# Kernel optimization log

Hardware: AMD Instinct MI355X
Metric: run time of the kernel (lower is better)

## Reference

```python
import jax, jax.numpy as jnp
import numpy as np

D_MODEL = 1024
D_STATE = 16
EXPAND = 2
D_CONV = 4
D_INNER = EXPAND * D_MODEL          # 2048
DT_RANK = D_MODEL // 16             # 64
B = 2
L = 1024
EPS = 1e-5


def setup_inputs() -> dict:
    key = jax.random.key(0)
    ks = jax.random.split(key, 8)
    s = 0.02
    return {
        "x": jax.random.normal(ks[0], (B, L, D_MODEL), jnp.float32),
        "ln_gamma": jnp.ones((D_MODEL,), jnp.float32),
        "ln_beta": jnp.zeros((D_MODEL,), jnp.float32),
        "in_proj_w": jax.random.normal(ks[1], (2 * D_INNER, D_MODEL), jnp.float32) * s,
        "conv_w": jax.random.normal(ks[2], (D_INNER, 1, D_CONV), jnp.float32) * s,
        "conv_b": jnp.zeros((D_INNER,), jnp.float32),
        "x_proj_w": jax.random.normal(ks[3], (DT_RANK + 2 * D_STATE, D_INNER), jnp.float32) * s,
        "dt_proj_w": jax.random.normal(ks[4], (D_INNER, DT_RANK), jnp.float32) * s,
        "dt_proj_b": jax.random.normal(ks[5], (D_INNER,), jnp.float32) * 0.01,
        "A_log": jnp.log(jnp.tile(jnp.arange(1, D_STATE + 1, dtype=jnp.float32), (D_INNER, 1))),
        "D_skip": jnp.ones((D_INNER,), jnp.float32),
        "out_proj_w": jax.random.normal(ks[6], (D_MODEL, D_INNER), jnp.float32) * s,
    }


def _layernorm(x, g, b):
    mu = jnp.mean(x, axis=-1, keepdims=True)
    var = jnp.mean((x - mu) ** 2, axis=-1, keepdims=True)
    return (x - mu) * jax.lax.rsqrt(var + EPS) * g + b


def _mamba_forward(x, ln_gamma, ln_beta, in_proj_w, conv_w, conv_b,
                   x_proj_w, dt_proj_w, dt_proj_b, A_log, D_skip, out_proj_w):
    residual = x
    xn = _layernorm(x, ln_gamma, ln_beta)

    # in_proj -> split into ssm input u and gate z   (b, l, 2*d_inner)
    xz = jnp.einsum('bld,ed->ble', xn, in_proj_w)
    u, z = jnp.split(xz, 2, axis=-1)

    # causal depthwise conv1d (padding = d_conv-1 on the left, truncated to L)
    uc = jnp.transpose(u, (0, 2, 1))  # (b, d_inner, l)
    uc = jax.lax.conv_general_dilated(
        uc, conv_w, window_strides=(1,), padding=[(D_CONV - 1, 0)],
        feature_group_count=D_INNER,
        dimension_numbers=('NCH', 'OIH', 'NCH'))
    uc = uc + conv_b[None, :, None]
    u = jax.nn.silu(jnp.transpose(uc, (0, 2, 1)))  # (b, l, d_inner)

    # selective SSM
    A = -jnp.exp(A_log)                              # (d_inner, d_state)
    x_dbl = jnp.einsum('bld,ed->ble', u, x_proj_w)   # (b, l, dt_rank+2*n)
    dt, Bm, Cm = jnp.split(x_dbl, [DT_RANK, DT_RANK + D_STATE], axis=-1)
    delta = jax.nn.softplus(jnp.einsum('blr,dr->bld', dt, dt_proj_w) + dt_proj_b)

    def step(h, inputs):
        d_t, B_t, C_t, u_t = inputs            # (b,di) (b,n) (b,n) (b,di)
        dA = jnp.exp(d_t[..., None] * A)       # (b, di, n)
        h = dA * h + (d_t * u_t)[..., None] * B_t[:, None, :]
        y = jnp.einsum('bdn,bn->bd', h, C_t)
        return h, y

    h0 = jnp.zeros((x.shape[0], D_INNER, D_STATE), x.dtype)
    xs = (jnp.moveaxis(delta, 1, 0), jnp.moveaxis(Bm, 1, 0),
          jnp.moveaxis(Cm, 1, 0), jnp.moveaxis(u, 1, 0))
    _, ys = jax.lax.scan(step, h0, xs)
    y = jnp.moveaxis(ys, 0, 1) + u * D_skip     # (b, l, d_inner)

    y = y * jax.nn.silu(z)                      # gated output
    out = jnp.einsum('ble,de->bld', y, out_proj_w)
    # dropout is identity in eval mode
    return out + residual


def reference(x, ln_gamma, ln_beta, in_proj_w, conv_w, conv_b,
              x_proj_w, dt_proj_w, dt_proj_b, A_log, D_skip, out_proj_w):
    return _mamba_forward(x, ln_gamma, ln_beta, in_proj_w, conv_w, conv_b,
                          x_proj_w, dt_proj_w, dt_proj_b, A_log, D_skip, out_proj_w)
```

## Files before the change

kernel.cpp:

```cpp
#include <hip/hip_runtime.h>

#define D_MODEL 1024
#define D_STATE 16
#define D_INNER 2048
#define DT_RANK 64
#define NBATCH 2
#define SEQ_L 1024
#define M_ROWS (NBATCH * SEQ_L)
#define CHUNK 32
#define NCHUNK (SEQ_L / CHUNK)

typedef __bf16 bf16x8 __attribute__((ext_vector_type(8)));
typedef float f32x4 __attribute__((ext_vector_type(4)));
typedef unsigned short u16;
typedef unsigned int u32;

__device__ __forceinline__ float bf2f(u16 h) {
    return __uint_as_float(((unsigned)h) << 16);
}
__device__ __forceinline__ u16 f2bf(float f) {
    unsigned u = __float_as_uint(f);
    u += 0x7fff + ((u >> 16) & 1);
    return (u16)(u >> 16);
}

__global__ __launch_bounds__(256) void prep(
    const float* __restrict__ s0, const float* __restrict__ s1,
    const float* __restrict__ s2, const float* __restrict__ s3,
    u16* __restrict__ d0, u16* __restrict__ d1,
    u16* __restrict__ d2, u16* __restrict__ d3,
    const float* __restrict__ x, const float* __restrict__ g,
    const float* __restrict__ b, u16* __restrict__ xn) {
    int blk = blockIdx.x;
    if (blk < 25856) {
        int idx = blk * 256 + threadIdx.x;
        if (idx < 4194304) {
            d0[idx] = f2bf(s0[idx]);
        } else if (idx < 6291456) {
            int i = idx - 4194304; d1[i] = f2bf(s1[i]);
        } else if (idx < 6488064) {
            int i = idx - 6291456; d2[i] = f2bf(s2[i]);
        } else {
            int i = idx - 6488064; d3[i] = f2bf(s3[i]);
        }
        return;
    }
    int row = blk - 25856;
    const float4* xr = (const float4*)(x + (size_t)row * D_MODEL);
    float4 v = xr[threadIdx.x];
    float s  = v.x + v.y + v.z + v.w;
    float ss = v.x * v.x + v.y * v.y + v.z * v.z + v.w * v.w;
#pragma unroll
    for (int off = 32; off > 0; off >>= 1) {
        s  += __shfl_down(s,  off, 64);
        ss += __shfl_down(ss, off, 64);
    }
    __shared__ float sh_s[4], sh_ss[4];
    int wid = threadIdx.x >> 6;
    if ((threadIdx.x & 63) == 0) { sh_s[wid] = s; sh_ss[wid] = ss; }
    __syncthreads();
    float mu  = (sh_s[0] + sh_s[1] + sh_s[2] + sh_s[3]) * (1.0f / D_MODEL);
    float var = (sh_ss[0] + sh_ss[1] + sh_ss[2] + sh_ss[3]) * (1.0f / D_MODEL) - mu * mu;
    float rs = rsqrtf(var + 1e-5f);
    int c0 = threadIdx.x * 4;
    float vv[4] = {v.x, v.y, v.z, v.w};
#pragma unroll
    for (int j = 0; j < 4; j++) {
        int c = c0 + j;
        float o = (vv[j] - mu) * rs * g[c] + b[c];
        xn[(size_t)row * D_MODEL + c] = f2bf(o);
    }
}

template <int BM, int BN, int WM, int WN, int MODE>
__global__ __launch_bounds__(256) void gemm_lds(
    const __bf16* __restrict__ A, const __bf16* __restrict__ W,
    int K, int Ksteps, int ldC,
    float* __restrict__ outF, u16* __restrict__ outB) {
    constexpr int WCOLS = BN / (WN * 16);
    __shared__ __bf16 As[BM * 32];
    __shared__ __bf16 Bs[BN * 32];
    int tid  = threadIdx.x;
    int lane = tid & 63;
    int wid  = tid >> 6;
    int l16  = lane & 15;
    int quad = lane >> 4;
    int wr = wid / WCOLS;
    int wc = wid % WCOLS;
    int m0 = blockIdx.y * BM;
    int n0 = blockIdx.x * BN;
    int kbase = blockIdx.z * Ksteps * 32;

    f32x4 acc[WM][WN];
#pragma unroll
    for (int mi = 0; mi < WM; mi++)
#pragma unroll
        for (int nj = 0; nj < WN; nj++)
            acc[mi][nj] = (f32x4){0.f, 0.f, 0.f, 0.f};

    for (int ki = 0; ki < Ksteps; ki++) {
        int k0 = kbase + ki * 32;
        __syncthreads();
#pragma unroll
        for (int i = 0; i < BM / 64; i++) {
            int t   = i * 256 + tid;
            int row = t >> 2;
            int cg  = (t & 3) ^ ((row >> 1) & 3);
            __builtin_amdgcn_global_load_lds(
                (const __attribute__((address_space(1))) u32*)(A + (size_t)(m0 + row) * K + k0 + cg * 8),
                (__attribute__((address_space(3))) u32*)(As + (i * 256 + wid * 64) * 8),
                16, 0, 0);
        }
#pragma unroll
        for (int i = 0; i < BN / 64; i++) {
            int t   = i * 256 + tid;
            int row = t >> 2;
            int cg  = (t & 3) ^ ((row >> 1) & 3);
            __builtin_amdgcn_global_load_lds(
                (const __attribute__((address_space(1))) u32*)(W + (size_t)(n0 + row) * K + k0 + cg * 8),
                (__attribute__((address_space(3))) u32*)(Bs + (i * 256 + wid * 64) * 8),
                16, 0, 0);
        }
        __syncthreads();

        bf16x8 af[WM], bfr[WN];
#pragma unroll
        for (int mi = 0; mi < WM; mi++) {
            int r  = wr * WM * 16 + mi * 16 + l16;
            int cg = quad ^ ((r >> 1) & 3);
            af[mi] = *(const bf16x8*)(As + r * 32 + cg * 8);
        }
#pragma unroll
        for (int nj = 0; nj < WN; nj++) {
            int r  = wc * WN * 16 + nj * 16 + l16;
            int cg = quad ^ ((r >> 1) & 3);
            bfr[nj] = *(const bf16x8*)(Bs + r * 32 + cg * 8);
        }
#pragma unroll
        for (int mi = 0; mi < WM; mi++)
#pragma unroll
            for (int nj = 0; nj < WN; nj++)
                acc[mi][nj] = __builtin_amdgcn_mfma_f32_16x16x32_bf16(
                    af[mi], bfr[nj], acc[mi][nj], 0, 0, 0);
    }

    float* outP = (MODE == 4) ? outF + (size_t)blockIdx.z * M_ROWS * ldC : outF;
#pragma unroll
    for (int mi = 0; mi < WM; mi++) {
#pragma unroll
        for (int nj = 0; nj < WN; nj++) {
            int col = n0 + wc * WN * 16 + nj * 16 + l16;
#pragma unroll
            for (int r = 0; r < 4; r++) {
                int row = m0 + wr * WM * 16 + mi * 16 + quad * 4 + r;
                float v = acc[mi][nj][r];
                if (MODE == 0) {
                    outB[(size_t)row * ldC + col] = f2bf(v);
                } else {
                    outP[(size_t)row * ldC + col] = v;
                }
            }
        }
    }
}

__global__ __launch_bounds__(256) void out_reduce(
    const float* __restrict__ p, const float* __restrict__ x,
    float* __restrict__ out) {
    int idx = blockIdx.x * 256 + threadIdx.x;
    const int N = M_ROWS * D_MODEL;
    float4 a = ((const float4*)p)[idx];
    float4 b = ((const float4*)(p + N))[idx];
    float4 c = ((const float4*)(p + 2 * N))[idx];
    float4 d = ((const float4*)(p + 3 * N))[idx];
    float4 r = ((const float4*)x)[idx];
    float4 o;
    o.x = a.x + b.x + c.x + d.x + r.x;
    o.y = a.y + b.y + c.y + d.y + r.y;
    o.z = a.z + b.z + c.z + d.z + r.z;
    o.w = a.w + b.w + c.w + d.w + r.w;
    ((float4*)out)[idx] = o;
}

template <int MODE>
__global__ __launch_bounds__(256) void gemm_bt(
    const __bf16* __restrict__ A, const __bf16* __restrict__ W,
    int K, int Ksplit, int Nw, int ldC,
    float* __restrict__ outF, u16* __restrict__ outB16,
    const float* __restrict__ auxF) {
    int lane = threadIdx.x & 63;
    int wid  = threadIdx.x >> 6;
    int m0 = blockIdx.y * 64;
    int n0 = blockIdx.x * 64;
    int kc = blockIdx.z;
    int l16  = lane & 15;
    int quad = lane >> 4;
    int mrow = m0 + wid * 16 + l16;

    const __bf16* ap = A + (size_t)mrow * K + kc * Ksplit + quad * 8;
    const __bf16* wp[4];
#pragma unroll
    for (int j = 0; j < 4; j++) {
        int nc = n0 + j * 16 + l16;
        if (nc > Nw - 1) nc = Nw - 1;
        wp[j] = W + (size_t)nc * K + kc * Ksplit + quad * 8;
    }
    f32x4 acc[4];
#pragma unroll
    for (int j = 0; j < 4; j++) acc[j] = (f32x4){0.f, 0.f, 0.f, 0.f};

    for (int k = 0; k < Ksplit; k += 32) {
        bf16x8 a = *(const bf16x8*)ap;
        ap += 32;
#pragma unroll
        for (int j = 0; j < 4; j++) {
            bf16x8 bfr = *(const bf16x8*)wp[j];
            wp[j] += 32;
            acc[j] = __builtin_amdgcn_mfma_f32_16x16x32_bf16(a, bfr, acc[j], 0, 0, 0);
        }
    }
    float* out = (MODE == 1) ? outF + (size_t)kc * (M_ROWS * 96) : outF;
#pragma unroll
    for (int j = 0; j < 4; j++) {
        int col = n0 + j * 16 + l16;
#pragma unroll
        for (int r = 0; r < 4; r++) {
            int row = m0 + wid * 16 + quad * 4 + r;
            float v = acc[j][r];
            if (MODE == 1) {
                if (col < Nw) out[(size_t)row * ldC + col] = v;
            } else {
                float t = v + auxF[col];
                float sp = (t > 20.f) ? t : log1pf(__expf(t));
                outB16[(size_t)row * ldC + col] = f2bf(sp);
            }
        }
    }
}

__global__ __launch_bounds__(256) void xdbl_reduce(
    const float* __restrict__ xdp, float* __restrict__ xd,
    u16* __restrict__ dtb) {
    int idx = blockIdx.x * 256 + threadIdx.x;
    const int N = M_ROWS * 96;
    float v = 0.f;
#pragma unroll
    for (int i = 0; i < 8; i++) v += xdp[idx + i * N];
    xd[idx] = v;
    int mrow = idx / 96;
    int r = idx - mrow * 96;
    if (r < DT_RANK) dtb[mrow * DT_RANK + r] = f2bf(v);
}

__global__ __launch_bounds__(256) void conv_silu(
    const u16* __restrict__ xz, const float* __restrict__ cw,
    const float* __restrict__ cb, u16* __restrict__ uc) {
    int idx = blockIdx.x * 256 + threadIdx.x;
    int d = idx & (D_INNER - 1);
    int m = idx >> 11;
    int t = m & (SEQ_L - 1);
    float s = cb[d];
#pragma unroll
    for (int j = 0; j < 4; j++) {
        int tt = t - 3 + j;
        if (tt >= 0) {
            s += cw[d * 4 + j] *
                 bf2f(xz[(size_t)(m - 3 + j) * (2 * D_INNER) + d]);
        }
    }
    float sig = 1.f / (1.f + __expf(-s));
    uc[idx] = f2bf(s * sig);
}

__global__ __launch_bounds__(256) void scan_chunk(
    const u16* __restrict__ delta, const u16* __restrict__ uc,
    const float* __restrict__ xd, const float* __restrict__ A_log,
    float* __restrict__ Pst, float* __restrict__ Sst) {
    __shared__ float Bsh[CHUNK][16];
    int tid  = threadIdx.x;
    int lane = tid & 63;
    int w    = tid >> 6;
    int dsub = lane & 15;
    int g    = lane >> 4;
    int n0   = g * 4;
    int c = blockIdx.x, b = blockIdx.z;
    int d = blockIdx.y * 64 + w * 16 + dsub;
    int mbase = b * SEQ_L + c * CHUNK;

    if (tid < CHUNK * 4) {
        int row = tid >> 2, q = tid & 3;
        *(float4*)&Bsh[row][q * 4] =
            *(const float4*)(xd + (size_t)(mbase + row) * 96 + DT_RANK + q * 4);
    }
    __syncthreads();

    float a[4];
    {
        float4 a0 = *(const float4*)(A_log + d * D_STATE + n0);
        a[0] = -__expf(a0.x); a[1] = -__expf(a0.y);
        a[2] = -__expf(a0.z); a[3] = -__expf(a0.w);
    }
    float P[4] = {1.f, 1.f, 1.f, 1.f}, S[4] = {0.f, 0.f, 0.f, 0.f};

    for (int t0 = 0; t0 < CHUNK; t0 += 4) {
        float dlv[4], uv[4];
#pragma unroll
        for (int i = 0; i < 4; i++) {
            int m = mbase + t0 + i;
            dlv[i] = bf2f(delta[(size_t)m * D_INNER + d]);
            uv[i]  = bf2f(uc[(size_t)m * D_INNER + d]);
        }
#pragma unroll
        for (int i = 0; i < 4; i++) {
            float c1 = dlv[i] * uv[i];
#pragma unroll
            for (int j = 0; j < 4; j++) {
                float dA = __expf(dlv[i] * a[j]);
                P[j] *= dA;
                S[j] = dA * S[j] + c1 * Bsh[t0 + i][n0 + j];
            }
        }
    }
    size_t s = ((size_t)(b * D_INNER + d) * NCHUNK + c) * D_STATE + n0;
    *(float4*)(Pst + s) = (float4){P[0], P[1], P[2], P[3]};
    *(float4*)(Sst + s) = (float4){S[0], S[1], S[2], S[3]};
}

__global__ __launch_bounds__(256) void scan_combine(
    const float* __restrict__ Pst, const float* __restrict__ Sst,
    float* __restrict__ Hin) {
    int idx = blockIdx.x * 256 + threadIdx.x;
    int bd = idx >> 4;
    int n  = idx & 15;
    float h = 0.f;
#pragma unroll
    for (int c = 0; c < NCHUNK; ++c) {
        size_t s = ((size_t)bd * NCHUNK + c) * D_STATE + n;
        Hin[s] = h;
        h = Pst[s] * h + Sst[s];
    }
}

__global__ __launch_bounds__(256) void scan_apply(
    const u16* __restrict__ delta, const u16* __restrict__ uc,
    const float* __restrict__ xd, const u16* __restrict__ xz,
    const float* __restrict__ A_log, const float* __restrict__ Dsk,
    const float* __restrict__ Hin, u16* __restrict__ yg) {
    __shared__ float BCs[CHUNK][32];
    int tid  = threadIdx.x;
    int lane = tid & 63;
    int w    = tid >> 6;
    int dsub = lane & 15;
    int g    = lane >> 4;
    int n0   = g * 4;
    int c = blockIdx.x, b = blockIdx.z;
    int d = blockIdx.y * 64 + w * 16 + dsub;
    int mbase = b * SEQ_L + c * CHUNK;

    {
        int row = tid >> 3, q = tid & 7;
        *(float4*)&BCs[row][q * 4] =
            *(const float4*)(xd + (size_t)(mbase + row) * 96 + DT_RANK + q * 4);
    }
    __syncthreads();

    float a[4];
    {
        float4 a0 = *(const float4*)(A_log + d * D_STATE + n0);
        a[0] = -__expf(a0.x); a[1] = -__expf(a0.y);
        a[2] = -__expf(a0.z); a[3] = -__expf(a0.w);
    }
    float h[4];
    {
        float4 h0 = *(const float4*)(Hin +
            (((size_t)(b * D_INNER + d) * NCHUNK + c) * D_STATE + n0));
        h[0] = h0.x; h[1] = h0.y; h[2] = h0.z; h[3] = h0.w;
    }
    float dsk = Dsk[d];

    for (int t0 = 0; t0 < CHUNK; t0 += 4) {
        float dlv[4], uv[4], zv[4];
#pragma unroll
        for (int i = 0; i < 4; i++) {
            int m = mbase + t0 + i;
            dlv[i] = bf2f(delta[(size_t)m * D_INNER + d]);
            uv[i]  = bf2f(uc[(size_t)m * D_INNER + d]);
            zv[i]  = bf2f(xz[(size_t)m * (2 * D_INNER) + D_INNER + d]);
        }
#pragma unroll
        for (int i = 0; i < 4; i++) {
            int t = t0 + i;
            float c1 = dlv[i] * uv[i];
            float y = 0.f;
#pragma unroll
            for (int j = 0; j < 4; j++) {
                float dA = __expf(dlv[i] * a[j]);
                h[j] = dA * h[j] + c1 * BCs[t][n0 + j];
                y += h[j] * BCs[t][16 + n0 + j];
            }
            y += __shfl_xor(y, 16);
            y += __shfl_xor(y, 32);
            if (g == 0) {
                float z = zv[i];
                float yv = y + uv[i] * dsk;
                float gt = z / (1.f + __expf(-z));
                yg[(size_t)(mbase + t) * D_INNER + d] = f2bf(yv * gt);
            }
        }
    }
}

extern "C" void kernel_launch(void* const* d_in, const int* in_sizes, int n_in,
                              void* d_out, int out_size, void* d_ws, size_t ws_size,
                              hipStream_t stream) {
    const float* x         = (const float*)d_in[0];
    const float* ln_g      = (const float*)d_in[1];
    const float* ln_b      = (const float*)d_in[2];
    const float* in_proj_w = (const float*)d_in[3];
    const float* conv_w    = (const float*)d_in[4];
    const float* conv_b    = (const float*)d_in[5];
    const float* x_proj_w  = (const float*)d_in[6];
    const float* dt_proj_w = (const float*)d_in[7];
    const float* dt_proj_b = (const float*)d_in[8];
    const float* A_log     = (const float*)d_in[9];
    const float* Dsk       = (const float*)d_in[10];
    const float* out_proj_w= (const float*)d_in[11];

    char* ws = (char*)d_ws;
    u16* xn   = (u16*)ws;    ws += (size_t)M_ROWS * D_MODEL * 2;
    u16* xz   = (u16*)ws;    ws += (size_t)M_ROWS * 2 * D_INNER * 2;
    u16* ucv  = (u16*)ws;    ws += (size_t)M_ROWS * D_INNER * 2;
    float* xd = (float*)ws;  ws += (size_t)M_ROWS * 96 * 4;
    u16* dtb  = (u16*)ws;    ws += (size_t)M_ROWS * DT_RANK * 2;
    u16* dl   = (u16*)ws;    ws += (size_t)M_ROWS * D_INNER * 2;
    u16* yg   = (u16*)ws;    ws += (size_t)M_ROWS * D_INNER * 2;
    u16* w_in = (u16*)ws;    ws += (size_t)4194304 * 2;
    u16* w_out= (u16*)ws;    ws += (size_t)2097152 * 2;
    u16* w_xp = (u16*)ws;    ws += (size_t)196608 * 2;
    u16* w_dt = (u16*)ws;    ws += (size_t)131072 * 2;
    float* Pst = (float*)ws; ws += (size_t)NBATCH * D_INNER * D_STATE * NCHUNK * 4;
    float* Sst = (float*)ws; ws += (size_t)NBATCH * D_INNER * D_STATE * NCHUNK * 4;
    float* Hin = (float*)ws; ws += (size_t)NBATCH * D_INNER * D_STATE * NCHUNK * 4;
    float* xdp = (float*)ws; ws += (size_t)8 * M_ROWS * 96 * 4;
    float* opart = (float*)ws;

    prep<<<25856 + M_ROWS, 256, 0, stream>>>(
        in_proj_w, out_proj_w, x_proj_w, dt_proj_w, w_in, w_out, w_xp, w_dt,
        x, ln_g, ln_b, xn);
    gemm_lds<64, 128, 4, 2, 0><<<dim3(4096 / 128, M_ROWS / 64, 1), 256, 0, stream>>>(
        (const __bf16*)xn, (const __bf16*)w_in, D_MODEL, D_MODEL / 32, 2 * D_INNER,
        nullptr, xz);
    conv_silu<<<(M_ROWS * D_INNER) / 256, 256, 0, stream>>>(xz, conv_w, conv_b, ucv);
    gemm_bt<1><<<dim3(2, 32, 8), 256, 0, stream>>>(
        (const __bf16*)ucv, (const __bf16*)w_xp, D_INNER, D_INNER / 8, 96, 96,
        xdp, nullptr, nullptr);
    xdbl_reduce<<<(M_ROWS * 96) / 256, 256, 0, stream>>>(xdp, xd, dtb);
    gemm_bt<2><<<dim3(32, 32, 1), 256, 0, stream>>>(
        (const __bf16*)dtb, (const __bf16*)w_dt, DT_RANK, DT_RANK, D_INNER,
        D_INNER, nullptr, dl, dt_proj_b);
    dim3 sgrid(NCHUNK, D_INNER / 64, NBATCH);
    scan_chunk<<<sgrid, 256, 0, stream>>>(dl, ucv, xd, A_log, Pst, Sst);
    scan_combine<<<(NBATCH * D_INNER * D_STATE) / 256, 256, 0, stream>>>(Pst, Sst, Hin);
    scan_apply<<<sgrid, 256, 0, stream>>>(dl, ucv, xd, xz, A_log, Dsk, Hin, yg);
    gemm_lds<64, 128, 4, 2, 4><<<dim3(1024 / 128, M_ROWS / 64, 4), 256, 0, stream>>>(
        (const __bf16*)yg, (const __bf16*)w_out, D_INNER, D_INNER / 4 / 32, D_MODEL,
        opart, nullptr);
    out_reduce<<<(M_ROWS * D_MODEL / 4) / 256, 256, 0, stream>>>(
        opart, x, (float*)d_out);
}
```

Before: 268.3 us.

## Vectorize weight conversion and conv_silu, enlarge GEMM M-tiles to 128

The weight fp32-to-bf16 conversion in prep now handles four elements per thread with float4 loads and 64-bit stores, which cuts the block count by four. conv_silu now handles eight channels per thread using 16-byte bf16 loads and stores. The in_proj and out_proj GEMMs switch from 64x128 to 128x128 tiles with a 4x4 warp layout to get more data reuse. Larger tiles halve the number of GEMM blocks, which may lower occupancy or wave balance on the grid.

Result: slower. 275.5 us (+2.7%).

```diff
diff --git a/kernel.cpp b/kernel.cpp
--- a/kernel.cpp
+++ b/kernel.cpp
@@ -14,6 +14,8 @@
 typedef float f32x4 __attribute__((ext_vector_type(4)));
 typedef unsigned short u16;
 typedef unsigned int u32;
+typedef u16 u16x4 __attribute__((ext_vector_type(4)));
+typedef u16 u16x8 __attribute__((ext_vector_type(8)));
 
 __device__ __forceinline__ float bf2f(u16 h) {
     return __uint_as_float(((unsigned)h) << 16);
@@ -32,20 +34,19 @@
     const float* __restrict__ x, const float* __restrict__ g,
     const float* __restrict__ b, u16* __restrict__ xn) {
     int blk = blockIdx.x;
-    if (blk < 25856) {
+    if (blk < 6464) {
         int idx = blk * 256 + threadIdx.x;
-        if (idx < 4194304) {
-            d0[idx] = f2bf(s0[idx]);
-        } else if (idx < 6291456) {
-            int i = idx - 4194304; d1[i] = f2bf(s1[i]);
-        } else if (idx < 6488064) {
-            int i = idx - 6291456; d2[i] = f2bf(s2[i]);
-        } else {
-            int i = idx - 6488064; d3[i] = f2bf(s3[i]);
-        }
+        const float4* s; u16* dp; int i;
+        if (idx < 1048576)      { s = (const float4*)s0; i = idx;           dp = d0; }
+        else if (idx < 1572864) { s = (const float4*)s1; i = idx - 1048576; dp = d1; }
+        else if (idx < 1622016) { s = (const float4*)s2; i = idx - 1572864; dp = d2; }
+        else                    { s = (const float4*)s3; i = idx - 1622016; dp = d3; }
+        float4 v = s[i];
+        u16x4 o = {f2bf(v.x), f2bf(v.y), f2bf(v.z), f2bf(v.w)};
+        *(u16x4*)(dp + (size_t)i * 4) = o;
         return;
     }
-    int row = blk - 25856;
+    int row = blk - 6464;
     const float4* xr = (const float4*)(x + (size_t)row * D_MODEL);
     float4 v = xr[threadIdx.x];
     float s  = v.x + v.y + v.z + v.w;
@@ -256,20 +257,35 @@
     const u16* __restrict__ xz, const float* __restrict__ cw,
     const float* __restrict__ cb, u16* __restrict__ uc) {
     int idx = blockIdx.x * 256 + threadIdx.x;
-    int d = idx & (D_INNER - 1);
-    int m = idx >> 11;
+    int base = idx * 8;
+    int d = base & (D_INNER - 1);
+    int m = base >> 11;
     int t = m & (SEQ_L - 1);
-    float s = cb[d];
+    float s[8];
+    {
+        float4 b0 = *(const float4*)(cb + d);
+        float4 b1 = *(const float4*)(cb + d + 4);
+        s[0] = b0.x; s[1] = b0.y; s[2] = b0.z; s[3] = b0.w;
+        s[4] = b1.x; s[5] = b1.y; s[6] = b1.z; s[7] = b1.w;
+    }
 #pragma unroll
     for (int j = 0; j < 4; j++) {
         int tt = t - 3 + j;
         if (tt >= 0) {
-            s += cw[d * 4 + j] *
-                 bf2f(xz[(size_t)(m - 3 + j) * (2 * D_INNER) + d]);
-        }
-    }
-    float sig = 1.f / (1.f + __expf(-s));
-    uc[idx] = f2bf(s * sig);
+            u16x8 uv = *(const u16x8*)(xz + (size_t)(m - 3 + j) * (2 * D_INNER) + d);
+#pragma unroll
+            for (int q = 0; q < 8; q++) {
+                s[q] += cw[(d + q) * 4 + j] * bf2f(uv[q]);
+            }
+        }
+    }
+    u16x8 o;
+#pragma unroll
+    for (int q = 0; q < 8; q++) {
+        float sig = 1.f / (1.f + __expf(-s[q]));
+        o[q] = f2bf(s[q] * sig);
+    }
+    *(u16x8*)(uc + base) = o;
 }
 
 __global__ __launch_bounds__(256) void scan_chunk(
@@ -444,13 +460,13 @@
     float* xdp = (float*)ws; ws += (size_t)8 * M_ROWS * 96 * 4;
     float* opart = (float*)ws;
 
-    prep<<<25856 + M_ROWS, 256, 0, stream>>>(
+    prep<<<6464 + M_ROWS, 256, 0, stream>>>(
         in_proj_w, out_proj_w, x_proj_w, dt_proj_w, w_in, w_out, w_xp, w_dt,
         x, ln_g, ln_b, xn);
-    gemm_lds<64, 128, 4, 2, 0><<<dim3(4096 / 128, M_ROWS / 64, 1), 256, 0, stream>>>(
+    gemm_lds<128, 128, 4, 4, 0><<<dim3(4096 / 128, M_ROWS / 128, 1), 256, 0, stream>>>(
         (const __bf16*)xn, (const __bf16*)w_in, D_MODEL, D_MODEL / 32, 2 * D_INNER,
         nullptr, xz);
-    conv_silu<<<(M_ROWS * D_INNER) / 256, 256, 0, stream>>>(xz, conv_w, conv_b, ucv);
+    conv_silu<<<(M_ROWS * D_INNER) / (256 * 8), 256, 0, stream>>>(xz, conv_w, conv_b, ucv);
     gemm_bt<1><<<dim3(2, 32, 8), 256, 0, stream>>>(
         (const __bf16*)ucv, (const __bf16*)w_xp, D_INNER, D_INNER / 8, 96, 96,
         xdp, nullptr, nullptr);
@@ -462,7 +478,7 @@
     scan_chunk<<<sgrid, 256, 0, stream>>>(dl, ucv, xd, A_log, Pst, Sst);
     scan_combine<<<(NBATCH * D_INNER * D_STATE) / 256, 256, 0, stream>>>(Pst, Sst, Hin);
     scan_apply<<<sgrid, 256, 0, stream>>>(dl, ucv, xd, xz, A_log, Dsk, Hin, yg);
-    gemm_lds<64, 128, 4, 2, 4><<<dim3(1024 / 128, M_ROWS / 64, 4), 256, 0, stream>>>(
+    gemm_lds<128, 128, 4, 4, 4><<<dim3(1024 / 128, M_ROWS / 128, 4), 256, 0, stream>>>(
         (const __bf16*)yg, (const __bf16*)w_out, D_INNER, D_INNER / 4 / 32, D_MODEL,
         opart, nullptr);
     out_reduce<<<(M_ROWS * D_MODEL / 4) / 256, 256, 0, stream>>>(
```
